# Performance work log

Hardware: AMD Instinct MI355X
Metric: run time of the kernel (lower is better)

## Reference

```python
import jax, jax.numpy as jnp
import numpy as np

FLOAT_MIN = -100000.0

def setup_inputs() -> dict:
    key = jax.random.key(0)
    ks = jax.random.split(key, 6)
    B, S, Q, K = 16, 8192, 1024, 256
    stdv = 1.0 / np.sqrt(K)
    return {
        "query": jax.random.normal(ks[0], (B, Q), dtype=jnp.float32),
        "keys": jax.random.normal(ks[1], (B, S, K), dtype=jnp.float32),
        "values": jax.random.normal(ks[2], (B, S, K), dtype=jnp.float32),
        "kv_mask": jnp.ones((B, S, 1), dtype=jnp.float32),
        "W_attr": jax.random.uniform(ks[3], (K, Q), jnp.float32, -stdv, stdv),
        "b_attr": jax.random.uniform(ks[4], (K,), jnp.float32, -stdv, stdv),
        "V_attr": jax.random.uniform(ks[5], (K,), jnp.float32, -stdv, stdv),
    }

def reference(query, keys, values, kv_mask, W_attr, b_attr, V_attr):
    # projected query: [B, 1, K]
    q = jnp.einsum('bq,kq->bk', query, W_attr)[:, None, :]
    # additive energies: [B, S, 1]
    energies = jnp.einsum('bsk,k->bs', jnp.tanh(keys + q + b_attr), V_attr)[:, :, None]
    energies = kv_mask * energies + (1.0 - kv_mask) * FLOAT_MIN
    scores = jax.nn.softmax(energies, axis=1)          # [B, S, 1]
    ctx = jnp.sum(values * scores, axis=1)             # [B, V_dim]
    return (scores, ctx)
```

## Files before the change

### kernel.cpp

```cpp
#include <hip/hip_runtime.h>
#include <math.h>

#define BB 16
#define SS 8192
#define KK 256
#define QQ 1024

static constexpr float C2L2E = 2.88539008177792681f;
static constexpr float L2E = 1.44269504088896341f;
static constexpr float FLOAT_MIN_V = -100000.0f;

typedef float floatx4 __attribute__((ext_vector_type(4)));

__device__ __forceinline__ float wave_sum(float v) {
#pragma unroll
  for (int off = 32; off >= 1; off >>= 1) v += __shfl_xor(v, off, 64);
  return v;
}

__device__ __forceinline__ float wave_max(float v) {
#pragma unroll
  for (int off = 32; off >= 1; off >>= 1) v = fmaxf(v, __shfl_xor(v, off, 64));
  return v;
}

__device__ __forceinline__ floatx4 ldnt(const float* p) {
  return __builtin_nontemporal_load((const floatx4*)p);
}

__global__ __launch_bounds__(256) void qproj_kernel(
    const float* __restrict__ query, const float* __restrict__ W,
    const float* __restrict__ b_attr, float* __restrict__ qb2) {
  const int blk = blockIdx.x;
  const int b = blk >> 6;
  const int kg = blk & 63;
  const int lane = threadIdx.x & 63;
  const int w = threadIdx.x >> 6;
  const int k = kg * 4 + w;

  const float4* q4 = (const float4*)(query + (size_t)b * QQ);
  const float4* w4 = (const float4*)(W + (size_t)k * QQ);
  float acc = 0.f;
#pragma unroll
  for (int j = 0; j < 4; ++j) {
    const float4 qv = q4[j * 64 + lane];
    const float4 wv = w4[j * 64 + lane];
    acc = fmaf(wv.x, qv.x, acc);
    acc = fmaf(wv.y, qv.y, acc);
    acc = fmaf(wv.z, qv.z, acc);
    acc = fmaf(wv.w, qv.w, acc);
  }
  acc = wave_sum(acc);
  if (lane == 0) qb2[b * KK + k] = C2L2E * (acc + b_attr[k]);
}

#define FROWS 64
__global__ __launch_bounds__(256) void fused_kernel(
    const float* __restrict__ keys, const float* __restrict__ values,
    const float* __restrict__ mask, const float* __restrict__ V_attr,
    const float* __restrict__ qb2, float* __restrict__ e,
    float* __restrict__ part_m, float* __restrict__ part_l,
    float* __restrict__ part_acc) {
  const int blk = blockIdx.x;
  const int b = blk / (SS / FROWS);
  const int lane = threadIdx.x & 63;
  const int w = threadIdx.x >> 6;
  const int s0 = (blk % (SS / FROWS)) * FROWS + w * (FROWS / 4);

  const float4 v4 = ((const float4*)V_attr)[lane];
  const float sv = wave_sum(v4.x + v4.y + v4.z + v4.w);
  const float4 nv2 =
      make_float4(-2.f * v4.x, -2.f * v4.y, -2.f * v4.z, -2.f * v4.w);
  const float4 qb = ((const float4*)qb2)[b * (KK / 4) + lane];

  const float* krow = keys + (size_t)(b * SS + s0) * KK;
  const float* vrow = values + (size_t)(b * SS + s0) * KK;
  floatx4 kf = ldnt(krow + 4 * lane);
  floatx4 vf = ldnt(vrow + 4 * lane);

  float m = -3.4e38f, l = 0.f;
  float4 acc = make_float4(0.f, 0.f, 0.f, 0.f);
  for (int i = 0; i < FROWS / 4; ++i) {
    const floatx4 ck = kf;
    const floatx4 cv = vf;
    if (i < FROWS / 4 - 1) {
      kf = ldnt(krow + (size_t)(i + 1) * KK + 4 * lane);
      vf = ldnt(vrow + (size_t)(i + 1) * KK + 4 * lane);
    }
    const float mk = mask[b * SS + s0 + i];
    float r0 = __builtin_amdgcn_rcpf(
        1.f + __builtin_amdgcn_exp2f(fmaf(ck.x, C2L2E, qb.x)));
    float r1 = __builtin_amdgcn_rcpf(
        1.f + __builtin_amdgcn_exp2f(fmaf(ck.y, C2L2E, qb.y)));
    float r2 = __builtin_amdgcn_rcpf(
        1.f + __builtin_amdgcn_exp2f(fmaf(ck.z, C2L2E, qb.z)));
    float r3 = __builtin_amdgcn_rcpf(
        1.f + __builtin_amdgcn_exp2f(fmaf(ck.w, C2L2E, qb.w)));
    float p = fmaf(nv2.x, r0, fmaf(nv2.y, r1, fmaf(nv2.z, r2, nv2.w * r3)));
    p = wave_sum(p);
    const float es = p + sv;
    const float x = mk * es + (1.f - mk) * FLOAT_MIN_V;
    if (lane == 0) e[b * SS + s0 + i] = x;
    const float newm = fmaxf(m, x);
    const float sc = __builtin_amdgcn_exp2f((m - newm) * L2E);
    const float pe = __builtin_amdgcn_exp2f((x - newm) * L2E);
    l = fmaf(l, sc, pe);
    acc.x = fmaf(acc.x, sc, pe * cv.x);
    acc.y = fmaf(acc.y, sc, pe * cv.y);
    acc.z = fmaf(acc.z, sc, pe * cv.z);
    acc.w = fmaf(acc.w, sc, pe * cv.w);
    m = newm;
  }

  __shared__ float lacc[4][KK];
  __shared__ float lm[4], ll[4];
  ((float4*)&lacc[w][0])[lane] = acc;
  if (lane == 0) {
    lm[w] = m;
    ll[w] = l;
  }
  __syncthreads();
  const float M = fmaxf(fmaxf(lm[0], lm[1]), fmaxf(lm[2], lm[3]));
  const float w0 = __builtin_amdgcn_exp2f((lm[0] - M) * L2E);
  const float w1 = __builtin_amdgcn_exp2f((lm[1] - M) * L2E);
  const float w2 = __builtin_amdgcn_exp2f((lm[2] - M) * L2E);
  const float w3 = __builtin_amdgcn_exp2f((lm[3] - M) * L2E);
  const int t = threadIdx.x;
  const float ca =
      fmaf(w0, lacc[0][t], fmaf(w1, lacc[1][t], fmaf(w2, lacc[2][t], w3 * lacc[3][t])));
  part_acc[(size_t)blk * KK + t] = ca;
  if (t == 0) {
    part_m[blk] = M;
    part_l[blk] = fmaf(w0, ll[0], fmaf(w1, ll[1], fmaf(w2, ll[2], w3 * ll[3])));
  }
}

__global__ __launch_bounds__(1024) void finalize_kernel(
    const float* __restrict__ part_m, const float* __restrict__ part_l,
    const float* __restrict__ part_acc, const float* __restrict__ e,
    float* __restrict__ scores, float* __restrict__ ctx) {
  const int b = blockIdx.x;
  const int tid = threadIdx.x;
  const int lane = tid & 63;
  constexpr int NP = SS / FROWS;
  __shared__ float sm[NP], sl[NP], sscale[NP];
  __shared__ float cred[4][KK];

  if (tid < NP) {
    sm[tid] = part_m[b * NP + tid];
    sl[tid] = part_l[b * NP + tid];
  }
  __syncthreads();

  const float M = wave_max(fmaxf(sm[lane], sm[lane + 64]));
  const float L = wave_sum(
      fmaf(__builtin_amdgcn_exp2f((sm[lane] - M) * L2E), sl[lane],
           __builtin_amdgcn_exp2f((sm[lane + 64] - M) * L2E) * sl[lane + 64]));
  if (tid < NP) sscale[tid] = __builtin_amdgcn_exp2f((sm[tid] - M) * L2E);
  __syncthreads();

  const int g = tid >> 8;
  const int k = tid & 255;
  float s = 0.f;
#pragma unroll 8
  for (int j = g * 32; j < g * 32 + 32; ++j)
    s = fmaf(sscale[j], part_acc[(size_t)(b * NP + j) * KK + k], s);
  cred[g][k] = s;
  __syncthreads();
  const float invL = 1.f / L;
  if (tid < KK)
    ctx[b * KK + tid] =
        (cred[0][tid] + cred[1][tid] + cred[2][tid] + cred[3][tid]) * invL;

#pragma unroll
  for (int i = 0; i < 8; ++i) {
    const int s_idx = tid + i * 1024;
    const float x = e[b * SS + s_idx];
    scores[b * SS + s_idx] = __builtin_amdgcn_exp2f((x - M) * L2E) * invL;
  }
}

extern "C" void kernel_launch(void* const* d_in, const int* in_sizes, int n_in,
                              void* d_out, int out_size, void* d_ws,
                              size_t ws_size, hipStream_t stream) {
  const float* query = (const float*)d_in[0];
  const float* keys = (const float*)d_in[1];
  const float* values = (const float*)d_in[2];
  const float* mask = (const float*)d_in[3];
  const float* W = (const float*)d_in[4];
  const float* b_attr = (const float*)d_in[5];
  const float* V_attr = (const float*)d_in[6];

  float* scores = (float*)d_out;
  float* ctx = scores + BB * SS;

  float* qb2 = (float*)d_ws;
  float* e = qb2 + BB * KK;
  float* part_m = e + BB * SS;
  float* part_l = part_m + BB * (SS / FROWS);
  float* part_acc = part_l + BB * (SS / FROWS);

  qproj_kernel<<<BB * (KK / 4), 256, 0, stream>>>(query, W, b_attr, qb2);
  fused_kernel<<<BB * (SS / FROWS), 256, 0, stream>>>(
      keys, values, mask, V_attr, qb2, e, part_m, part_l, part_acc);
  finalize_kernel<<<BB, 1024, 0, stream>>>(part_m, part_l, part_acc, e,
                                           scores, ctx);
}
```

Before: 276.1 us.

## Drop online softmax max tracking and process two rows per iteration

Removes the running-max rescaling from the streaming softmax. Unnormalised exp(energy) values are stored, and partial sums are combined by plain addition in the block reduction and the finalize kernel. This relies on the energies being bounded, since tanh is bounded and the energy magnitude is at most sum|V_attr|. The main loop also handles two rows per iteration, interleaving the two wave reductions to add ILP. The trade-off is overflow risk for large V_attr and a division by zero when every position is masked.

```diff
diff --git a/kernel.cpp b/kernel.cpp
--- a/kernel.cpp
+++ b/kernel.cpp
@@ -15,12 +15,6 @@
 __device__ __forceinline__ float wave_sum(float v) {
 #pragma unroll
   for (int off = 32; off >= 1; off >>= 1) v += __shfl_xor(v, off, 64);
-  return v;
-}
-
-__device__ __forceinline__ float wave_max(float v) {
-#pragma unroll
-  for (int off = 32; off >= 1; off >>= 1) v = fmaxf(v, __shfl_xor(v, off, 64));
   return v;
 }
 
@@ -58,9 +52,8 @@
 __global__ __launch_bounds__(256) void fused_kernel(
     const float* __restrict__ keys, const float* __restrict__ values,
     const float* __restrict__ mask, const float* __restrict__ V_attr,
-    const float* __restrict__ qb2, float* __restrict__ e,
-    float* __restrict__ part_m, float* __restrict__ part_l,
-    float* __restrict__ part_acc) {
+    const float* __restrict__ qb2, float* __restrict__ pbuf,
+    float* __restrict__ part_l, float* __restrict__ part_acc) {
   const int blk = blockIdx.x;
   const int b = blk / (SS / FROWS);
   const int lane = threadIdx.x & 63;
@@ -75,99 +68,112 @@
 
   const float* krow = keys + (size_t)(b * SS + s0) * KK;
   const float* vrow = values + (size_t)(b * SS + s0) * KK;
-  floatx4 kf = ldnt(krow + 4 * lane);
-  floatx4 vf = ldnt(vrow + 4 * lane);
-
-  float m = -3.4e38f, l = 0.f;
-  float4 acc = make_float4(0.f, 0.f, 0.f, 0.f);
-  for (int i = 0; i < FROWS / 4; ++i) {
-    const floatx4 ck = kf;
-    const floatx4 cv = vf;
-    if (i < FROWS / 4 - 1) {
-      kf = ldnt(krow + (size_t)(i + 1) * KK + 4 * lane);
-      vf = ldnt(vrow + (size_t)(i + 1) * KK + 4 * lane);
-    }
-    const float mk = mask[b * SS + s0 + i];
-    float r0 = __builtin_amdgcn_rcpf(
-        1.f + __builtin_amdgcn_exp2f(fmaf(ck.x, C2L2E, qb.x)));
-    float r1 = __builtin_amdgcn_rcpf(
-        1.f + __builtin_amdgcn_exp2f(fmaf(ck.y, C2L2E, qb.y)));
-    float r2 = __builtin_amdgcn_rcpf(
-        1.f + __builtin_amdgcn_exp2f(fmaf(ck.z, C2L2E, qb.z)));
-    float r3 = __builtin_amdgcn_rcpf(
-        1.f + __builtin_amdgcn_exp2f(fmaf(ck.w, C2L2E, qb.w)));
-    float p = fmaf(nv2.x, r0, fmaf(nv2.y, r1, fmaf(nv2.z, r2, nv2.w * r3)));
-    p = wave_sum(p);
-    const float es = p + sv;
-    const float x = mk * es + (1.f - mk) * FLOAT_MIN_V;
-    if (lane == 0) e[b * SS + s0 + i] = x;
-    const float newm = fmaxf(m, x);
-    const float sc = __builtin_amdgcn_exp2f((m - newm) * L2E);
-    const float pe = __builtin_amdgcn_exp2f((x - newm) * L2E);
-    l = fmaf(l, sc, pe);
-    acc.x = fmaf(acc.x, sc, pe * cv.x);
-    acc.y = fmaf(acc.y, sc, pe * cv.y);
-    acc.z = fmaf(acc.z, sc, pe * cv.z);
-    acc.w = fmaf(acc.w, sc, pe * cv.w);
-    m = newm;
+  floatx4 kf0 = ldnt(krow + 4 * lane);
+  floatx4 vf0 = ldnt(vrow + 4 * lane);
+  floatx4 kf1 = ldnt(krow + KK + 4 * lane);
+  floatx4 vf1 = ldnt(vrow + KK + 4 * lane);
+
+  float l0 = 0.f, l1 = 0.f;
+  float4 acc0 = make_float4(0.f, 0.f, 0.f, 0.f);
+  float4 acc1 = make_float4(0.f, 0.f, 0.f, 0.f);
+  for (int i = 0; i < FROWS / 4; i += 2) {
+    const floatx4 ck0 = kf0, cv0 = vf0, ck1 = kf1, cv1 = vf1;
+    if (i + 2 < FROWS / 4) {
+      kf0 = ldnt(krow + (size_t)(i + 2) * KK + 4 * lane);
+      vf0 = ldnt(vrow + (size_t)(i + 2) * KK + 4 * lane);
+      kf1 = ldnt(krow + (size_t)(i + 3) * KK + 4 * lane);
+      vf1 = ldnt(vrow + (size_t)(i + 3) * KK + 4 * lane);
+    }
+    const float mk0 = mask[b * SS + s0 + i];
+    const float mk1 = mask[b * SS + s0 + i + 1];
+
+    float p0, p1;
+    {
+      float a0 = __builtin_amdgcn_rcpf(
+          1.f + __builtin_amdgcn_exp2f(fmaf(ck0.x, C2L2E, qb.x)));
+      float a1 = __builtin_amdgcn_rcpf(
+          1.f + __builtin_amdgcn_exp2f(fmaf(ck0.y, C2L2E, qb.y)));
+      float a2 = __builtin_amdgcn_rcpf(
+          1.f + __builtin_amdgcn_exp2f(fmaf(ck0.z, C2L2E, qb.z)));
+      float a3 = __builtin_amdgcn_rcpf(
+          1.f + __builtin_amdgcn_exp2f(fmaf(ck0.w, C2L2E, qb.w)));
+      p0 = fmaf(nv2.x, a0, fmaf(nv2.y, a1, fmaf(nv2.z, a2, nv2.w * a3)));
+    }
+    {
+      float a0 = __builtin_amdgcn_rcpf(
+          1.f + __builtin_amdgcn_exp2f(fmaf(ck1.x, C2L2E, qb.x)));
+      float a1 = __builtin_amdgcn_rcpf(
+          1.f + __builtin_amdgcn_exp2f(fmaf(ck1.y, C2L2E, qb.y)));
+      float a2 = __builtin_amdgcn_rcpf(
+          1.f + __builtin_amdgcn_exp2f(fmaf(ck1.z, C2L2E, qb.z)));
+      float a3 = __builtin_amdgcn_rcpf(
+          1.f + __builtin_amdgcn_exp2f(fmaf(ck1.w, C2L2E, qb.w)));
+      p1 = fmaf(nv2.x, a0, fmaf(nv2.y, a1, fmaf(nv2.z, a2, nv2.w * a3)));
+    }
+#pragma unroll
+    for (int off = 32; off >= 1; off >>= 1) {
+      p0 += __shfl_xor(p0, off, 64);
+      p1 += __shfl_xor(p1, off, 64);
+    }
+    const float x0 = mk0 * (p0 + sv) + (1.f - mk0) * FLOAT_MIN_V;
+    const float x1 = mk1 * (p1 + sv) + (1.f - mk1) * FLOAT_MIN_V;
+    const float pe0 = __builtin_amdgcn_exp2f(x0 * L2E);
+    const float pe1 = __builtin_amdgcn_exp2f(x1 * L2E);
+    if (lane == 0) {
+      pbuf[b * SS + s0 + i] = pe0;
+      pbuf[b * SS + s0 + i + 1] = pe1;
+    }
+    l0 += pe0;
+    l1 += pe1;
+    acc0.x = fmaf(pe0, cv0.x, acc0.x);
+    acc0.y = fmaf(pe0, cv0.y, acc0.y);
+    acc0.z = fmaf(pe0, cv0.z, acc0.z);
+    acc0.w = fmaf(pe0, cv0.w, acc0.w);
+    acc1.x = fmaf(pe1, cv1.x, acc1.x);
+    acc1.y = fmaf(pe1, cv1.y, acc1.y);
+    acc1.z = fmaf(pe1, cv1.z, acc1.z);
+    acc1.w = fmaf(pe1, cv1.w, acc1.w);
   }
+  const float l = l0 + l1;
+  const float4 acc = make_float4(acc0.x + acc1.x, acc0.y + acc1.y,
+                                 acc0.z + acc1.z, acc0.w + acc1.w);
 
   __shared__ float lacc[4][KK];
-  __shared__ float lm[4], ll[4];
+  __shared__ float ll[4];
   ((float4*)&lacc[w][0])[lane] = acc;
-  if (lane == 0) {
-    lm[w] = m;
-    ll[w] = l;
-  }
+  if (lane == 0) ll[w] = l;
   __syncthreads();
-  const float M = fmaxf(fmaxf(lm[0], lm[1]), fmaxf(lm[2], lm[3]));
-  const float w0 = __builtin_amdgcn_exp2f((lm[0] - M) * L2E);
-  const float w1 = __builtin_amdgcn_exp2f((lm[1] - M) * L2E);
-  const float w2 = __builtin_amdgcn_exp2f((lm[2] - M) * L2E);
-  const float w3 = __builtin_amdgcn_exp2f((lm[3] - M) * L2E);
   const int t = threadIdx.x;
-  const float ca =
-      fmaf(w0, lacc[0][t], fmaf(w1, lacc[1][t], fmaf(w2, lacc[2][t], w3 * lacc[3][t])));
-  part_acc[(size_t)blk * KK + t] = ca;
-  if (t == 0) {
-    part_m[blk] = M;
-    part_l[blk] = fmaf(w0, ll[0], fmaf(w1, ll[1], fmaf(w2, ll[2], w3 * ll[3])));
-  }
+  part_acc[(size_t)blk * KK + t] =
+      lacc[0][t] + lacc[1][t] + lacc[2][t] + lacc[3][t];
+  if (t == 0) part_l[blk] = ll[0] + ll[1] + ll[2] + ll[3];
 }
 
 __global__ __launch_bounds__(1024) void finalize_kernel(
-    const float* __restrict__ part_m, const float* __restrict__ part_l,
-    const float* __restrict__ part_acc, const float* __restrict__ e,
-    float* __restrict__ scores, float* __restrict__ ctx) {
+    const float* __restrict__ part_l, const float* __restrict__ part_acc,
+    const float* __restrict__ pbuf, float* __restrict__ scores,
+    float* __restrict__ ctx) {
   const int b = blockIdx.x;
   const int tid = threadIdx.x;
   const int lane = tid & 63;
   constexpr int NP = SS / FROWS;
-  __shared__ float sm[NP], sl[NP], sscale[NP];
+  __shared__ float sl[NP];
   __shared__ float cred[4][KK];
 
-  if (tid < NP) {
-    sm[tid] = part_m[b * NP + tid];
-    sl[tid] = part_l[b * NP + tid];
-  }
+  if (tid < NP) sl[tid] = part_l[b * NP + tid];
   __syncthreads();
 
-  const float M = wave_max(fmaxf(sm[lane], sm[lane + 64]));
-  const float L = wave_sum(
-      fmaf(__builtin_amdgcn_exp2f((sm[lane] - M) * L2E), sl[lane],
-           __builtin_amdgcn_exp2f((sm[lane + 64] - M) * L2E) * sl[lane + 64]));
-  if (tid < NP) sscale[tid] = __builtin_amdgcn_exp2f((sm[tid] - M) * L2E);
-  __syncthreads();
+  const float L = wave_sum(sl[lane] + sl[lane + 64]);
+  const float invL = 1.f / L;
 
   const int g = tid >> 8;
   const int k = tid & 255;
   float s = 0.f;
 #pragma unroll 8
   for (int j = g * 32; j < g * 32 + 32; ++j)
-    s = fmaf(sscale[j], part_acc[(size_t)(b * NP + j) * KK + k], s);
+    s += part_acc[(size_t)(b * NP + j) * KK + k];
   cred[g][k] = s;
   __syncthreads();
-  const float invL = 1.f / L;
   if (tid < KK)
     ctx[b * KK + tid] =
         (cred[0][tid] + cred[1][tid] + cred[2][tid] + cred[3][tid]) * invL;
@@ -175,8 +181,7 @@
 #pragma unroll
   for (int i = 0; i < 8; ++i) {
     const int s_idx = tid + i * 1024;
-    const float x = e[b * SS + s_idx];
-    scores[b * SS + s_idx] = __builtin_amdgcn_exp2f((x - M) * L2E) * invL;
+    scores[b * SS + s_idx] = pbuf[b * SS + s_idx] * invL;
   }
 }
 
@@ -195,14 +200,13 @@
   float* ctx = scores + BB * SS;
 
   float* qb2 = (float*)d_ws;
-  float* e = qb2 + BB * KK;
-  float* part_m = e + BB * SS;
-  float* part_l = part_m + BB * (SS / FROWS);
+  float* pbuf = qb2 + BB * KK;
+  float* part_l = pbuf + BB * SS;
   float* part_acc = part_l + BB * (SS / FROWS);
 
   qproj_kernel<<<BB * (KK / 4), 256, 0, stream>>>(query, W, b_attr, qb2);
   fused_kernel<<<BB * (SS / FROWS), 256, 0, stream>>>(
-      keys, values, mask, V_attr, qb2, e, part_m, part_l, part_acc);
-  finalize_kernel<<<BB, 1024, 0, stream>>>(part_m, part_l, part_acc, e,
-                                           scores, ctx);
-}
+      keys, values, mask, V_attr, qb2, pbuf, part_l, part_acc);
+  finalize_kernel<<<BB, 1024, 0, stream>>>(part_l, part_acc, pbuf, scores,
+                                           ctx);
+}
```

Result: no change. 273.1 us (-1.1%).
